# Optimization experiments

Hardware: AMD Instinct MI355X
Metric: run time of the kernel (lower is better)

Reference implementation:

```python
import jax, jax.numpy as jnp
import numpy as np

N, D_IN, D_HID, N_EXPERTS, TOP_K = 16384, 2048, 2048, 8, 2


def setup_inputs() -> dict:
    key = jax.random.key(0)
    k1, k2, k3, k4, k5 = jax.random.split(key, 5)
    x = jax.random.normal(k1, (N, D_IN), dtype=jnp.float32)
    W_experts = jax.random.normal(k2, (N_EXPERTS, D_IN, D_HID), dtype=jnp.float32) * 0.02
    b_experts = jax.random.normal(k3, (N_EXPERTS, D_HID), dtype=jnp.float32) * 0.02
    W_gate = jax.random.normal(k4, (D_IN, N_EXPERTS), dtype=jnp.float32) * 0.02
    b_gate = jax.random.normal(k5, (N_EXPERTS,), dtype=jnp.float32) * 0.02
    return {"x": x, "W_experts": W_experts, "b_experts": b_experts,
            "W_gate": W_gate, "b_gate": b_gate}


def reference(x, W_experts, b_experts, W_gate, b_gate):
    # gating softmax over experts: [N, E]
    gates = jax.nn.softmax(x @ W_gate + b_gate, axis=-1)
    # per-token top-k scores/indices: [N, K]
    top_scores, top_idx = jax.lax.top_k(gates, TOP_K)
    # FAITHFUL to original: experts chosen by the FIRST token's indices for all tokens
    idx0 = top_idx[0]                       # [K]
    W_sel = W_experts[idx0]                 # [K, D_IN, D_HID]
    b_sel = b_experts[idx0]                 # [K, D_HID]
    expert_out = jnp.einsum('ni,kio->nko', x, W_sel) + b_sel[None]  # [N, K, D_HID]
    # weight by each token's own top-k scores and sum over the K experts
    return (expert_out * top_scores[:, :, None]).sum(axis=1)        # [N, D_HID]
```

## Files before the change

kernel.cpp:

```cpp
#include <hip/hip_runtime.h>
#include <hip/hip_bf16.h>
#include <stdint.h>

#define N_TOK 16384
#define D_IN  2048
#define D_HID 2048

typedef __attribute__((ext_vector_type(8))) short  bf16x8;
typedef __attribute__((ext_vector_type(4))) float  f32x4;
typedef __attribute__((ext_vector_type(8))) unsigned short u16x8;

__device__ __forceinline__ unsigned short f2bf(float f) {
    unsigned int u = __float_as_uint(f);
    u = (u + 0x7FFFu + ((u >> 16) & 1u)) >> 16;
    return (unsigned short)u;
}

__global__ void gate_kernel(const float* __restrict__ x,
                            const float* __restrict__ Wg,
                            const float* __restrict__ bg,
                            float* __restrict__ s12,
                            int* __restrict__ eidx) {
    const int token = blockIdx.x * 4 + (threadIdx.x >> 6);
    const int lane  = threadIdx.x & 63;
    const float* xr = x + (size_t)token * D_IN;

    float acc[8];
#pragma unroll
    for (int e = 0; e < 8; ++e) acc[e] = 0.f;

    for (int i = lane; i < D_IN; i += 64) {
        float xv = xr[i];
        const float4* wr = (const float4*)(Wg + (size_t)i * 8);
        float4 w0 = wr[0], w1 = wr[1];
        acc[0] += xv * w0.x; acc[1] += xv * w0.y;
        acc[2] += xv * w0.z; acc[3] += xv * w0.w;
        acc[4] += xv * w1.x; acc[5] += xv * w1.y;
        acc[6] += xv * w1.z; acc[7] += xv * w1.w;
    }
#pragma unroll
    for (int off = 32; off > 0; off >>= 1) {
#pragma unroll
        for (int e = 0; e < 8; ++e) acc[e] += __shfl_xor(acc[e], off);
    }

    float lg[8];
    float mx = -1e30f;
#pragma unroll
    for (int e = 0; e < 8; ++e) { lg[e] = acc[e] + bg[e]; mx = fmaxf(mx, lg[e]); }
    float sum = 0.f;
#pragma unroll
    for (int e = 0; e < 8; ++e) { lg[e] = expf(lg[e] - mx); sum += lg[e]; }
    float inv = 1.f / sum;

    float s1 = -1.f, s2 = -1.f; int i1 = 0, i2 = 0;
#pragma unroll
    for (int e = 0; e < 8; ++e) {
        float g = lg[e] * inv;
        if (g > s1)      { s2 = s1; i2 = i1; s1 = g; i1 = e; }
        else if (g > s2) { s2 = g;  i2 = e; }
    }
    if (lane == 0) {
        s12[token * 2]     = s1;
        s12[token * 2 + 1] = s2;
        if (token == 0) { eidx[0] = i1; eidx[1] = i2; }
    }
}

__global__ __launch_bounds__(256) void xconv_kernel(
    const float* __restrict__ x, unsigned short* __restrict__ xb) {
    const int mt = blockIdx.x >> 6;
    const int kt = blockIdx.x & 63;
    const int t  = threadIdx.x;
    const float* src = x + ((size_t)(mt * 256 + t)) * D_IN + kt * 32;
    unsigned short* slab = xb + ((size_t)(mt * 64 + kt)) * 8192;
#pragma unroll
    for (int ks = 0; ks < 4; ++ks) {
        float4 a = *(const float4*)(src + ks * 8);
        float4 b = *(const float4*)(src + ks * 8 + 4);
        u16x8 v;
        v[0] = f2bf(a.x); v[1] = f2bf(a.y); v[2] = f2bf(a.z); v[3] = f2bf(a.w);
        v[4] = f2bf(b.x); v[5] = f2bf(b.y); v[6] = f2bf(b.z); v[7] = f2bf(b.w);
        *(u16x8*)(slab + (ks * 256 + t) * 8) = v;
    }
}

__global__ void wconv_kernel(const float* __restrict__ W,
                             const int* __restrict__ eidx,
                             unsigned short* __restrict__ wbT) {
    __shared__ float tile[64][65];
    const int be  = blockIdx.z;
    const int e   = eidx[be];
    const int k0  = blockIdx.y * 64;
    const int n0  = blockIdx.x * 64;
    const int bx  = n0 >> 7;
    const int cl0 = n0 & 127;
    const int kt0 = k0 >> 5;
    const float* src = W + (size_t)e * D_IN * D_HID;
    const int t = threadIdx.x;

#pragma unroll
    for (int p = 0; p < 4; ++p) {
        int row = p * 16 + (t >> 4);
        int col = (t & 15) * 4;
        const float* s = src + (size_t)(k0 + row) * D_HID + n0 + col;
        tile[row][col]     = s[0];
        tile[row][col + 1] = s[1];
        tile[row][col + 2] = s[2];
        tile[row][col + 3] = s[3];
    }
    __syncthreads();

    const int g   = (t >> 5) * 8;
    const int ktl = t >> 7;
    const int ks  = (t >> 5) & 3;
#pragma unroll
    for (int p = 0; p < 2; ++p) {
        int n = p * 32 + (t & 31);
        u16x8 v;
#pragma unroll
        for (int j = 0; j < 8; ++j) v[j] = f2bf(tile[g + j][n]);
        unsigned short* dst = wbT + ((size_t)(bx * 64 + kt0 + ktl)) * 8192 +
                              ((size_t)(ks * 256 + be * 128 + cl0 + n)) * 8;
        *(u16x8*)dst = v;
    }
}

#define GLD16(gp, lp)                                                        \
    __builtin_amdgcn_global_load_lds(                                        \
        (const __attribute__((address_space(1))) void*)(gp),                 \
        (__attribute__((address_space(3))) void*)(lp), 16, 0, 0)

#define LDSV(SLOT) (*(const bf16x8*)&lds[(SLOT) * 8])

#define STAGE_A(SBAS, KT)                                                    \
    do {                                                                     \
        GLD16(gA0 + (size_t)(KT) * 8192,        &lds[((SBAS) + t512) * 8]);  \
        GLD16(gA0 + (size_t)(KT) * 8192 + 4096, &lds[((SBAS) + 512 + t512) * 8]); \
    } while (0)
#define STAGE_B(SBAS, KT)                                                    \
    do {                                                                     \
        GLD16(gB0 + (size_t)(KT) * 8192,        &lds[((SBAS) + 1024 + t512) * 8]); \
        GLD16(gB0 + (size_t)(KT) * 8192 + 4096, &lds[((SBAS) + 1536 + t512) * 8]); \
    } while (0)

#define MF(MI, AV)                                                                              \
    acc[MI][0] = __builtin_amdgcn_mfma_f32_16x16x32_bf16(AV, bf0, acc[MI][0], 0, 0, 0);         \
    acc[MI][1] = __builtin_amdgcn_mfma_f32_16x16x32_bf16(AV, bf1, acc[MI][1], 0, 0, 0);         \
    acc[MI][2] = __builtin_amdgcn_mfma_f32_16x16x32_bf16(AV, bf2, acc[MI][2], 0, 0, 0);         \
    acc[MI][3] = __builtin_amdgcn_mfma_f32_16x16x32_bf16(AV, bf3, acc[MI][3], 0, 0, 0);

#define TILE(RB, SB, KT, DO_STAGE, VMSTR)                                    \
    do {                                                                     \
        const int rbas  = (RB) * 2048;                                       \
        const int abase = rbas + aks + arow;                                 \
        const int bbase = rbas + 1024 + aks + brow;                          \
        bf16x8 bf0 = LDSV(bbase), bf1 = LDSV(bbase + 16),                    \
               bf2 = LDSV(bbase + 32), bf3 = LDSV(bbase + 48);               \
        bf16x8 a0 = LDSV(abase), a1 = LDSV(abase + 16),                      \
               a2 = LDSV(abase + 32), a3 = LDSV(abase + 48);                 \
        bf16x8 a4 = LDSV(abase + 64), a5 = LDSV(abase + 80),                 \
               a6 = LDSV(abase + 96), a7 = LDSV(abase + 112);                \
        __builtin_amdgcn_s_barrier();                                        \
        if (DO_STAGE) STAGE_A((SB) * 2048, KT);                              \
        __builtin_amdgcn_s_setprio(1);                                       \
        MF(0, a0) MF(1, a1) MF(2, a2) MF(3, a3)                              \
        __builtin_amdgcn_s_setprio(0);                                       \
        asm volatile(VMSTR ::: "memory");                                    \
        __builtin_amdgcn_s_barrier();                                        \
        if (DO_STAGE) STAGE_B((SB) * 2048, KT);                              \
        __builtin_amdgcn_s_setprio(1);                                       \
        MF(4, a4) MF(5, a5) MF(6, a6) MF(7, a7)                              \
        __builtin_amdgcn_s_setprio(0);                                       \
    } while (0)

__global__ __launch_bounds__(512, 2) void moe_gemm_kernel(
    const unsigned short* __restrict__ xb,
    const unsigned short* __restrict__ wbT,
    const float* __restrict__ b_exp,
    const int* __restrict__ eidx,
    const float* __restrict__ s12,
    float* __restrict__ out) {
    __shared__ __align__(16) short lds[4 * 2048 * 8];

    const int t512 = threadIdx.x;
    const int lane = t512 & 63;
    const int w    = t512 >> 6;
    const int wm   = w >> 2;
    const int wn   = w & 3;

    const int bid = blockIdx.x;
    const int xcd = bid & 7;
    const int jb  = bid >> 3;
    const int bx  = xcd * 2 + (jb & 1);
    const int by  = jb >> 1;
    const int mbase = by * 256;
    const int nbase = bx * 128;

    const unsigned short* gA0 = xb  + ((size_t)by * 64) * 8192 + t512 * 8;
    const unsigned short* gB0 = wbT + ((size_t)bx * 64) * 8192 + t512 * 8;

    const int aks  = (lane >> 4) * 256;
    const int arow = wm * 128 + (lane & 15);
    const int brow = wn * 64 + (lane & 15);

    f32x4 acc[8][4];
#pragma unroll
    for (int mi = 0; mi < 8; ++mi)
#pragma unroll
        for (int ni = 0; ni < 4; ++ni) acc[mi][ni] = (f32x4){0.f, 0.f, 0.f, 0.f};

    STAGE_A(0, 0);    STAGE_B(0, 0);
    STAGE_A(2048, 1); STAGE_B(2048, 1);
    STAGE_A(4096, 2); STAGE_B(4096, 2);
    asm volatile("s_waitcnt vmcnt(8)" ::: "memory");
    __builtin_amdgcn_s_barrier();

#pragma unroll 4
    for (int t = 0; t < 61; ++t) {
        TILE(t & 3, (t + 3) & 3, t + 3, 1, "s_waitcnt vmcnt(6)");
    }
    TILE(1, 0, 0, 0, "s_waitcnt vmcnt(4)");
    TILE(2, 0, 0, 0, "s_waitcnt vmcnt(0)");
    TILE(3, 0, 0, 0, "s_waitcnt vmcnt(0)");

    __syncthreads();
    float* fl = (float*)lds;
    if (wn >= 2) {
        float* reg = fl + (wm * 2 + (wn - 2)) * 8192;
#pragma unroll
        for (int mi = 0; mi < 8; ++mi)
#pragma unroll
            for (int ni = 0; ni < 4; ++ni)
#pragma unroll
                for (int j = 0; j < 4; ++j) {
                    int row_l = mi * 16 + ((lane >> 4) << 2) + j;
                    int col_l = ni * 16 + (lane & 15);
                    reg[row_l * 64 + col_l] = acc[mi][ni][j];
                }
    }
    __syncthreads();
    if (wn < 2) {
        const float* reg = fl + (wm * 2 + wn) * 8192;
        const int e0 = eidx[0], e1 = eidx[1];
        const float* bb0 = b_exp + (size_t)e0 * D_HID;
        const float* bb1 = b_exp + (size_t)e1 * D_HID;
        const float2* s12v = (const float2*)s12;
        int   cc[4];
        float b0c[4], b1c[4];
#pragma unroll
        for (int ni = 0; ni < 4; ++ni) {
            cc[ni]  = nbase + wn * 64 + ni * 16 + (lane & 15);
            b0c[ni] = bb0[cc[ni]];
            b1c[ni] = bb1[cc[ni]];
        }
#pragma unroll
        for (int mi = 0; mi < 8; ++mi)
#pragma unroll
            for (int j = 0; j < 4; ++j) {
                int row_l = mi * 16 + ((lane >> 4) << 2) + j;
                int r = mbase + wm * 128 + row_l;
                float2 s = s12v[r];
#pragma unroll
                for (int ni = 0; ni < 4; ++ni) {
                    float y1 = reg[row_l * 64 + ni * 16 + (lane & 15)];
                    out[(size_t)r * D_HID + cc[ni]] =
                        s.x * (acc[mi][ni][j] + b0c[ni]) + s.y * (y1 + b1c[ni]);
                }
            }
    }
}

extern "C" void kernel_launch(void* const* d_in, const int* in_sizes, int n_in,
                              void* d_out, int out_size, void* d_ws, size_t ws_size,
                              hipStream_t stream) {
    const float* x         = (const float*)d_in[0];
    const float* W_experts = (const float*)d_in[1];
    const float* b_experts = (const float*)d_in[2];
    const float* W_gate    = (const float*)d_in[3];
    const float* b_gate    = (const float*)d_in[4];
    float* out = (float*)d_out;

    char* ws = (char*)d_ws;
    float* s12  = (float*)ws;
    int*   eidx = (int*)(ws + 131072);
    unsigned short* xb  = (unsigned short*)(ws + 262144);
    unsigned short* wbT = (unsigned short*)(ws + 262144 + 67108864);

    gate_kernel<<<N_TOK / 4, 256, 0, stream>>>(x, W_gate, b_gate, s12, eidx);
    xconv_kernel<<<4096, 256, 0, stream>>>(x, xb);
    wconv_kernel<<<dim3(32, 32, 2), 256, 0, stream>>>(W_experts, eidx, wbT);
    moe_gemm_kernel<<<1024, 512, 0, stream>>>(xb, wbT, b_experts, eidx, s12, out);
}
```

Before: 323.0 us.

## Software-pipeline LDS fragment loads across K-tiles with one barrier per tile

Restructures the GEMM main loop so the A/B fragment reads for the next K-tile are issued from LDS during the current tile's second MFMA phase, with double-buffered register sets. The per-tile barriers drop from two to one, and each phase issues its global staging before its MFMA block. The aim is to hide LDS read latency and barrier stalls behind MFMA work. The cost is more live VGPRs, which at 512 threads with two blocks per CU may cause spills. The tighter vmcnt and barrier ordering also risks races on LDS slot reuse.

```diff
diff --git a/kernel.cpp b/kernel.cpp
--- a/kernel.cpp
+++ b/kernel.cpp
@@ -144,34 +144,44 @@
         GLD16(gB0 + (size_t)(KT) * 8192 + 4096, &lds[((SBAS) + 1536 + t512) * 8]); \
     } while (0)
 
-#define MF(MI, AV)                                                                              \
-    acc[MI][0] = __builtin_amdgcn_mfma_f32_16x16x32_bf16(AV, bf0, acc[MI][0], 0, 0, 0);         \
-    acc[MI][1] = __builtin_amdgcn_mfma_f32_16x16x32_bf16(AV, bf1, acc[MI][1], 0, 0, 0);         \
-    acc[MI][2] = __builtin_amdgcn_mfma_f32_16x16x32_bf16(AV, bf2, acc[MI][2], 0, 0, 0);         \
-    acc[MI][3] = __builtin_amdgcn_mfma_f32_16x16x32_bf16(AV, bf3, acc[MI][3], 0, 0, 0);
-
-#define TILE(RB, SB, KT, DO_STAGE, VMSTR)                                    \
+#define MF16(ASET, BSET, MB)                                                 \
+    _Pragma("unroll")                                                        \
+    for (int mi = 0; mi < 4; ++mi)                                           \
+        _Pragma("unroll")                                                    \
+        for (int ni = 0; ni < 4; ++ni)                                       \
+            acc[(MB) + mi][ni] = __builtin_amdgcn_mfma_f32_16x16x32_bf16(    \
+                ASET[mi], BSET[ni], acc[(MB) + mi][ni], 0, 0, 0);
+
+#define PH1(TT, STG, AS, BS)                                                 \
     do {                                                                     \
-        const int rbas  = (RB) * 2048;                                       \
-        const int abase = rbas + aks + arow;                                 \
-        const int bbase = rbas + 1024 + aks + brow;                          \
-        bf16x8 bf0 = LDSV(bbase), bf1 = LDSV(bbase + 16),                    \
-               bf2 = LDSV(bbase + 32), bf3 = LDSV(bbase + 48);               \
-        bf16x8 a0 = LDSV(abase), a1 = LDSV(abase + 16),                      \
-               a2 = LDSV(abase + 32), a3 = LDSV(abase + 48);                 \
-        bf16x8 a4 = LDSV(abase + 64), a5 = LDSV(abase + 80),                 \
-               a6 = LDSV(abase + 96), a7 = LDSV(abase + 112);                \
+        const int rb = ((TT) & 3) * 2048;                                    \
+        a4[0] = LDSV(rb + aks + arow + 64);                                  \
+        a4[1] = LDSV(rb + aks + arow + 80);                                  \
+        a4[2] = LDSV(rb + aks + arow + 96);                                  \
+        a4[3] = LDSV(rb + aks + arow + 112);                                 \
+        if (STG) STAGE_A((((TT) + 3) & 3) * 2048, (TT) + 3);                 \
+        __builtin_amdgcn_s_setprio(1);                                       \
+        MF16(AS, BS, 0)                                                      \
+        __builtin_amdgcn_s_setprio(0);                                       \
+    } while (0)
+
+#define PH2(TT, STG, VMSTR, BN, AN, BC)                                      \
+    do {                                                                     \
+        const int rb = (((TT) + 1) & 3) * 2048;                              \
+        BN[0] = LDSV(rb + 1024 + aks + brow);                                \
+        BN[1] = LDSV(rb + 1024 + aks + brow + 16);                           \
+        BN[2] = LDSV(rb + 1024 + aks + brow + 32);                           \
+        BN[3] = LDSV(rb + 1024 + aks + brow + 48);                           \
+        AN[0] = LDSV(rb + aks + arow);                                       \
+        AN[1] = LDSV(rb + aks + arow + 16);                                  \
+        AN[2] = LDSV(rb + aks + arow + 32);                                  \
+        AN[3] = LDSV(rb + aks + arow + 48);                                  \
+        if (STG) STAGE_B((((TT) + 3) & 3) * 2048, (TT) + 3);                 \
+        asm volatile(VMSTR ::: "memory");                                    \
+        __builtin_amdgcn_s_setprio(1);                                       \
+        MF16(a4, BC, 4)                                                      \
+        __builtin_amdgcn_s_setprio(0);                                       \
         __builtin_amdgcn_s_barrier();                                        \
-        if (DO_STAGE) STAGE_A((SB) * 2048, KT);                              \
-        __builtin_amdgcn_s_setprio(1);                                       \
-        MF(0, a0) MF(1, a1) MF(2, a2) MF(3, a3)                              \
-        __builtin_amdgcn_s_setprio(0);                                       \
-        asm volatile(VMSTR ::: "memory");                                    \
-        __builtin_amdgcn_s_barrier();                                        \
-        if (DO_STAGE) STAGE_B((SB) * 2048, KT);                              \
-        __builtin_amdgcn_s_setprio(1);                                       \
-        MF(4, a4) MF(5, a5) MF(6, a6) MF(7, a7)                              \
-        __builtin_amdgcn_s_setprio(0);                                       \
     } while (0)
 
 __global__ __launch_bounds__(512, 2) void moe_gemm_kernel(
@@ -210,19 +220,39 @@
 #pragma unroll
         for (int ni = 0; ni < 4; ++ni) acc[mi][ni] = (f32x4){0.f, 0.f, 0.f, 0.f};
 
+    bf16x8 bA[4], a0A[4], bB[4], a0B[4], a4[4];
+
     STAGE_A(0, 0);    STAGE_B(0, 0);
     STAGE_A(2048, 1); STAGE_B(2048, 1);
     STAGE_A(4096, 2); STAGE_B(4096, 2);
-    asm volatile("s_waitcnt vmcnt(8)" ::: "memory");
+    asm volatile("s_waitcnt vmcnt(4)" ::: "memory");
     __builtin_amdgcn_s_barrier();
-
-#pragma unroll 4
-    for (int t = 0; t < 61; ++t) {
-        TILE(t & 3, (t + 3) & 3, t + 3, 1, "s_waitcnt vmcnt(6)");
-    }
-    TILE(1, 0, 0, 0, "s_waitcnt vmcnt(4)");
-    TILE(2, 0, 0, 0, "s_waitcnt vmcnt(0)");
-    TILE(3, 0, 0, 0, "s_waitcnt vmcnt(0)");
+    bA[0] = LDSV(1024 + aks + brow);      bA[1] = LDSV(1024 + aks + brow + 16);
+    bA[2] = LDSV(1024 + aks + brow + 32); bA[3] = LDSV(1024 + aks + brow + 48);
+    a0A[0] = LDSV(aks + arow);            a0A[1] = LDSV(aks + arow + 16);
+    a0A[2] = LDSV(aks + arow + 32);       a0A[3] = LDSV(aks + arow + 48);
+
+    for (int t = 0; t < 60; t += 2) {
+        PH1(t, 1, a0A, bA);
+        PH2(t, 1, "s_waitcnt vmcnt(4)", bB, a0B, bA);
+        PH1(t + 1, 1, a0B, bB);
+        PH2(t + 1, 1, "s_waitcnt vmcnt(4)", bA, a0A, bB);
+    }
+    PH1(60, 1, a0A, bA);
+    PH2(60, 1, "s_waitcnt vmcnt(4)", bB, a0B, bA);
+    PH1(61, 0, a0B, bB);
+    PH2(61, 0, "s_waitcnt vmcnt(0)", bA, a0A, bB);
+    PH1(62, 0, a0A, bA);
+    PH2(62, 0, "s_waitcnt vmcnt(0)", bB, a0B, bA);
+    {
+        const int rb = 3 * 2048;
+        a4[0] = LDSV(rb + aks + arow + 64);
+        a4[1] = LDSV(rb + aks + arow + 80);
+        a4[2] = LDSV(rb + aks + arow + 96);
+        a4[3] = LDSV(rb + aks + arow + 112);
+        MF16(a0B, bB, 0)
+        MF16(a4, bB, 4)
+    }
 
     __syncthreads();
     float* fl = (float*)lds;
```

After: 329.1 us. Within noise of the previous version (+1.9%).

## Restructure GEMM main loop into double-buffered four-phase pipeline

Applied to the files above, without the earlier changes.

Replaces the four-slot LDS ring of k-tiles with a double buffer of two-k-tile chunks, processed in four phases per iteration. Each phase loads a quarter of the A fragments (B fragments every other phase), issues the global-to-LDS prefetch for the matching slice of the next chunk, then runs 16 MFMAs behind a barrier and an explicit lgkmcnt wait. The aim is to spread LDS reads and global loads more evenly between MFMA bursts and to cut register pressure from holding eight A fragments at once. In exchange there are more barriers per k-tile and the prefetch distance is shorter than the previous three-tile lookahead.

```diff
diff --git a/kernel.cpp b/kernel.cpp
--- a/kernel.cpp
+++ b/kernel.cpp
@@ -133,45 +133,41 @@
 
 #define LDSV(SLOT) (*(const bf16x8*)&lds[(SLOT) * 8])
 
-#define STAGE_A(SBAS, KT)                                                    \
+#define PHASE(CB, P, T1, DOSTAGE, VMSTR)                                     \
     do {                                                                     \
-        GLD16(gA0 + (size_t)(KT) * 8192,        &lds[((SBAS) + t512) * 8]);  \
-        GLD16(gA0 + (size_t)(KT) * 8192 + 4096, &lds[((SBAS) + 512 + t512) * 8]); \
-    } while (0)
-#define STAGE_B(SBAS, KT)                                                    \
-    do {                                                                     \
-        GLD16(gB0 + (size_t)(KT) * 8192,        &lds[((SBAS) + 1024 + t512) * 8]); \
-        GLD16(gB0 + (size_t)(KT) * 8192 + 4096, &lds[((SBAS) + 1536 + t512) * 8]); \
-    } while (0)
-
-#define MF(MI, AV)                                                                              \
-    acc[MI][0] = __builtin_amdgcn_mfma_f32_16x16x32_bf16(AV, bf0, acc[MI][0], 0, 0, 0);         \
-    acc[MI][1] = __builtin_amdgcn_mfma_f32_16x16x32_bf16(AV, bf1, acc[MI][1], 0, 0, 0);         \
-    acc[MI][2] = __builtin_amdgcn_mfma_f32_16x16x32_bf16(AV, bf2, acc[MI][2], 0, 0, 0);         \
-    acc[MI][3] = __builtin_amdgcn_mfma_f32_16x16x32_bf16(AV, bf3, acc[MI][3], 0, 0, 0);
-
-#define TILE(RB, SB, KT, DO_STAGE, VMSTR)                                    \
-    do {                                                                     \
-        const int rbas  = (RB) * 2048;                                       \
-        const int abase = rbas + aks + arow;                                 \
-        const int bbase = rbas + 1024 + aks + brow;                          \
-        bf16x8 bf0 = LDSV(bbase), bf1 = LDSV(bbase + 16),                    \
-               bf2 = LDSV(bbase + 32), bf3 = LDSV(bbase + 48);               \
-        bf16x8 a0 = LDSV(abase), a1 = LDSV(abase + 16),                      \
-               a2 = LDSV(abase + 32), a3 = LDSV(abase + 48);                 \
-        bf16x8 a4 = LDSV(abase + 64), a5 = LDSV(abase + 80),                 \
-               a6 = LDSV(abase + 96), a7 = LDSV(abase + 112);                \
+        const int hb = (CB) * 4096 + ((P) >> 1) * 2048;                      \
+        if (((P) & 1) == 0) {                                                \
+            bC[0] = LDSV(hb + 1024 + bro);                                   \
+            bC[1] = LDSV(hb + 1024 + bro + 16);                              \
+            bC[2] = LDSV(hb + 1024 + bro + 32);                              \
+            bC[3] = LDSV(hb + 1024 + bro + 48);                              \
+        }                                                                    \
+        aP[0] = LDSV(hb + aro + ((P) & 1) * 64);                             \
+        aP[1] = LDSV(hb + aro + ((P) & 1) * 64 + 16);                        \
+        aP[2] = LDSV(hb + aro + ((P) & 1) * 64 + 32);                        \
+        aP[3] = LDSV(hb + aro + ((P) & 1) * 64 + 48);                        \
+        if (DOSTAGE) {                                                       \
+            const size_t so = ((size_t)(2 * (T1) + ((P) >> 1)) * 1024 +      \
+                               ((P) & 1) * 512) * 8;                         \
+            const int dd = ((CB) ^ 1) * 4096 + ((P) >> 1) * 2048 +           \
+                           ((P) & 1) * 512 + t512;                           \
+            GLD16(gA0 + so, &lds[dd * 8]);                                   \
+            GLD16(gB0 + so, &lds[(dd + 1024) * 8]);                          \
+        }                                                                    \
+        if (VMSTR[0]) asm volatile(VMSTR ::: "memory");                      \
         __builtin_amdgcn_s_barrier();                                        \
-        if (DO_STAGE) STAGE_A((SB) * 2048, KT);                              \
+        asm volatile("s_waitcnt lgkmcnt(0)" ::: "memory");                   \
+        __builtin_amdgcn_sched_barrier(0);                                   \
         __builtin_amdgcn_s_setprio(1);                                       \
-        MF(0, a0) MF(1, a1) MF(2, a2) MF(3, a3)                              \
+        _Pragma("unroll")                                                    \
+        for (int mi = 0; mi < 4; ++mi)                                       \
+            _Pragma("unroll")                                                \
+            for (int ni = 0; ni < 4; ++ni)                                   \
+                acc[((P) & 1) * 4 + mi][ni] =                                \
+                    __builtin_amdgcn_mfma_f32_16x16x32_bf16(                 \
+                        aP[mi], bC[ni], acc[((P) & 1) * 4 + mi][ni], 0, 0, 0); \
         __builtin_amdgcn_s_setprio(0);                                       \
-        asm volatile(VMSTR ::: "memory");                                    \
         __builtin_amdgcn_s_barrier();                                        \
-        if (DO_STAGE) STAGE_B((SB) * 2048, KT);                              \
-        __builtin_amdgcn_s_setprio(1);                                       \
-        MF(4, a4) MF(5, a5) MF(6, a6) MF(7, a7)                              \
-        __builtin_amdgcn_s_setprio(0);                                       \
     } while (0)
 
 __global__ __launch_bounds__(512, 2) void moe_gemm_kernel(
@@ -181,7 +177,7 @@
     const int* __restrict__ eidx,
     const float* __restrict__ s12,
     float* __restrict__ out) {
-    __shared__ __align__(16) short lds[4 * 2048 * 8];
+    __shared__ __align__(16) short lds[2 * 4096 * 8];
 
     const int t512 = threadIdx.x;
     const int lane = t512 & 63;
@@ -200,9 +196,8 @@
     const unsigned short* gA0 = xb  + ((size_t)by * 64) * 8192 + t512 * 8;
     const unsigned short* gB0 = wbT + ((size_t)bx * 64) * 8192 + t512 * 8;
 
-    const int aks  = (lane >> 4) * 256;
-    const int arow = wm * 128 + (lane & 15);
-    const int brow = wn * 64 + (lane & 15);
+    const int aro = (lane >> 4) * 256 + wm * 128 + (lane & 15);
+    const int bro = (lane >> 4) * 256 + wn * 64 + (lane & 15);
 
     f32x4 acc[8][4];
 #pragma unroll
@@ -210,19 +205,30 @@
 #pragma unroll
         for (int ni = 0; ni < 4; ++ni) acc[mi][ni] = (f32x4){0.f, 0.f, 0.f, 0.f};
 
-    STAGE_A(0, 0);    STAGE_B(0, 0);
-    STAGE_A(2048, 1); STAGE_B(2048, 1);
-    STAGE_A(4096, 2); STAGE_B(4096, 2);
-    asm volatile("s_waitcnt vmcnt(8)" ::: "memory");
+    bf16x8 aP[4], bC[4];
+
+#pragma unroll
+    for (int p = 0; p < 4; ++p) {
+        const size_t so = ((size_t)(p >> 1) * 1024 + (p & 1) * 512) * 8;
+        const int dd = (p >> 1) * 2048 + (p & 1) * 512 + t512;
+        GLD16(gA0 + so, &lds[dd * 8]);
+        GLD16(gB0 + so, &lds[(dd + 1024) * 8]);
+    }
+    asm volatile("s_waitcnt vmcnt(4)" ::: "memory");
     __builtin_amdgcn_s_barrier();
 
-#pragma unroll 4
-    for (int t = 0; t < 61; ++t) {
-        TILE(t & 3, (t + 3) & 3, t + 3, 1, "s_waitcnt vmcnt(6)");
-    }
-    TILE(1, 0, 0, 0, "s_waitcnt vmcnt(4)");
-    TILE(2, 0, 0, 0, "s_waitcnt vmcnt(0)");
-    TILE(3, 0, 0, 0, "s_waitcnt vmcnt(0)");
+    int cb = 0;
+    for (int t = 0; t < 31; ++t) {
+        PHASE(cb, 0, t + 1, 1, "");
+        PHASE(cb, 1, t + 1, 1, "s_waitcnt vmcnt(4)");
+        PHASE(cb, 2, t + 1, 1, "");
+        PHASE(cb, 3, t + 1, 1, "s_waitcnt vmcnt(4)");
+        cb ^= 1;
+    }
+    PHASE(1, 0, 0, 0, "");
+    PHASE(1, 1, 0, 0, "s_waitcnt vmcnt(0)");
+    PHASE(1, 2, 0, 0, "");
+    PHASE(1, 3, 0, 0, "");
 
     __syncthreads();
     float* fl = (float*)lds;
```

Measured after the change: 341.4 us. 1.06x slower.

## Load B fragments directly into registers, staging only A through LDS

Applied to the files above, without the earlier changes.

The GEMM main loop now streams only the A (token) tile through LDS with async global-to-LDS loads. Each wave loads its B (weight) fragments straight from global memory into registers, double-buffered one k-tile ahead. This halves LDS traffic and usage per stage and replaces two barriers per tile with one. The cost is more register pressure, per-wave redundant global loads of B across the wm waves, and reliance on carefully tuned vmcnt waits for correctness.

```diff
diff --git a/kernel.cpp b/kernel.cpp
--- a/kernel.cpp
+++ b/kernel.cpp
@@ -133,46 +133,38 @@
 
 #define LDSV(SLOT) (*(const bf16x8*)&lds[(SLOT) * 8])
 
-#define STAGE_A(SBAS, KT)                                                    \
+#define STAGE_A(SB, KT)                                                      \
     do {                                                                     \
-        GLD16(gA0 + (size_t)(KT) * 8192,        &lds[((SBAS) + t512) * 8]);  \
-        GLD16(gA0 + (size_t)(KT) * 8192 + 4096, &lds[((SBAS) + 512 + t512) * 8]); \
+        GLD16(gA0 + (size_t)(KT) * 8192,        &lds[((SB) * 1024 + t512) * 8]); \
+        GLD16(gA0 + (size_t)(KT) * 8192 + 4096, &lds[((SB) * 1024 + 512 + t512) * 8]); \
     } while (0)
-#define STAGE_B(SBAS, KT)                                                    \
+
+#define TILE(RB, STGT, DOSTG, BT, DOB, BC, BN, VMSTR, DOBAR)                 \
     do {                                                                     \
-        GLD16(gB0 + (size_t)(KT) * 8192,        &lds[((SBAS) + 1024 + t512) * 8]); \
-        GLD16(gB0 + (size_t)(KT) * 8192 + 4096, &lds[((SBAS) + 1536 + t512) * 8]); \
+        bf16x8 a[8];                                                         \
+        _Pragma("unroll")                                                    \
+        for (int mi = 0; mi < 8; ++mi)                                       \
+            a[mi] = LDSV((RB) * 1024 + abase + mi * 16);                     \
+        if (DOB) {                                                           \
+            const unsigned short* bp = gBfrag + (size_t)(BT) * 8192;         \
+            _Pragma("unroll")                                                \
+            for (int ni = 0; ni < 4; ++ni)                                   \
+                BN[ni] = *(const bf16x8*)(bp + ni * 128);                    \
+        }                                                                    \
+        if (DOSTG) STAGE_A((STGT) & 3, STGT);                                \
+        if (VMSTR[0]) asm volatile(VMSTR ::: "memory");                      \
+        __builtin_amdgcn_s_setprio(1);                                       \
+        _Pragma("unroll")                                                    \
+        for (int mi = 0; mi < 8; ++mi)                                       \
+            _Pragma("unroll")                                                \
+            for (int ni = 0; ni < 4; ++ni)                                   \
+                acc[mi][ni] = __builtin_amdgcn_mfma_f32_16x16x32_bf16(       \
+                    a[mi], BC[ni], acc[mi][ni], 0, 0, 0);                    \
+        __builtin_amdgcn_s_setprio(0);                                       \
+        if (DOBAR) __builtin_amdgcn_s_barrier();                             \
     } while (0)
 
-#define MF(MI, AV)                                                                              \
-    acc[MI][0] = __builtin_amdgcn_mfma_f32_16x16x32_bf16(AV, bf0, acc[MI][0], 0, 0, 0);         \
-    acc[MI][1] = __builtin_amdgcn_mfma_f32_16x16x32_bf16(AV, bf1, acc[MI][1], 0, 0, 0);         \
-    acc[MI][2] = __builtin_amdgcn_mfma_f32_16x16x32_bf16(AV, bf2, acc[MI][2], 0, 0, 0);         \
-    acc[MI][3] = __builtin_amdgcn_mfma_f32_16x16x32_bf16(AV, bf3, acc[MI][3], 0, 0, 0);
-
-#define TILE(RB, SB, KT, DO_STAGE, VMSTR)                                    \
-    do {                                                                     \
-        const int rbas  = (RB) * 2048;                                       \
-        const int abase = rbas + aks + arow;                                 \
-        const int bbase = rbas + 1024 + aks + brow;                          \
-        bf16x8 bf0 = LDSV(bbase), bf1 = LDSV(bbase + 16),                    \
-               bf2 = LDSV(bbase + 32), bf3 = LDSV(bbase + 48);               \
-        bf16x8 a0 = LDSV(abase), a1 = LDSV(abase + 16),                      \
-               a2 = LDSV(abase + 32), a3 = LDSV(abase + 48);                 \
-        bf16x8 a4 = LDSV(abase + 64), a5 = LDSV(abase + 80),                 \
-               a6 = LDSV(abase + 96), a7 = LDSV(abase + 112);                \
-        __builtin_amdgcn_s_barrier();                                        \
-        if (DO_STAGE) STAGE_A((SB) * 2048, KT);                              \
-        __builtin_amdgcn_s_setprio(1);                                       \
-        MF(0, a0) MF(1, a1) MF(2, a2) MF(3, a3)                              \
-        __builtin_amdgcn_s_setprio(0);                                       \
-        asm volatile(VMSTR ::: "memory");                                    \
-        __builtin_amdgcn_s_barrier();                                        \
-        if (DO_STAGE) STAGE_B((SB) * 2048, KT);                              \
-        __builtin_amdgcn_s_setprio(1);                                       \
-        MF(4, a4) MF(5, a5) MF(6, a6) MF(7, a7)                              \
-        __builtin_amdgcn_s_setprio(0);                                       \
-    } while (0)
+#define VM12 "s_waitcnt vmcnt(12)"
 
 __global__ __launch_bounds__(512, 2) void moe_gemm_kernel(
     const unsigned short* __restrict__ xb,
@@ -181,7 +173,7 @@
     const int* __restrict__ eidx,
     const float* __restrict__ s12,
     float* __restrict__ out) {
-    __shared__ __align__(16) short lds[4 * 2048 * 8];
+    __shared__ __align__(16) short lds[8192 * 8];
 
     const int t512 = threadIdx.x;
     const int lane = t512 & 63;
@@ -197,12 +189,12 @@
     const int mbase = by * 256;
     const int nbase = bx * 128;
 
-    const unsigned short* gA0 = xb  + ((size_t)by * 64) * 8192 + t512 * 8;
-    const unsigned short* gB0 = wbT + ((size_t)bx * 64) * 8192 + t512 * 8;
-
-    const int aks  = (lane >> 4) * 256;
-    const int arow = wm * 128 + (lane & 15);
-    const int brow = wn * 64 + (lane & 15);
+    const unsigned short* gA0 = xb + ((size_t)by * 64) * 8192 + t512 * 8;
+    const unsigned short* gBfrag =
+        wbT + ((size_t)bx * 64) * 8192 +
+        ((size_t)((lane >> 4) * 256 + wn * 64 + (lane & 15))) * 8;
+
+    const int abase = (lane >> 4) * 256 + wm * 128 + (lane & 15);
 
     f32x4 acc[8][4];
 #pragma unroll
@@ -210,19 +202,31 @@
 #pragma unroll
         for (int ni = 0; ni < 4; ++ni) acc[mi][ni] = (f32x4){0.f, 0.f, 0.f, 0.f};
 
-    STAGE_A(0, 0);    STAGE_B(0, 0);
-    STAGE_A(2048, 1); STAGE_B(2048, 1);
-    STAGE_A(4096, 2); STAGE_B(4096, 2);
+    bf16x8 b0[4], b1[4];
+
+    STAGE_A(0, 0);
+    STAGE_A(1, 1);
+    STAGE_A(2, 2);
+#pragma unroll
+    for (int ni = 0; ni < 4; ++ni)
+        b0[ni] = *(const bf16x8*)(gBfrag + ni * 128);
     asm volatile("s_waitcnt vmcnt(8)" ::: "memory");
     __builtin_amdgcn_s_barrier();
 
-#pragma unroll 4
-    for (int t = 0; t < 61; ++t) {
-        TILE(t & 3, (t + 3) & 3, t + 3, 1, "s_waitcnt vmcnt(6)");
-    }
-    TILE(1, 0, 0, 0, "s_waitcnt vmcnt(4)");
-    TILE(2, 0, 0, 0, "s_waitcnt vmcnt(0)");
-    TILE(3, 0, 0, 0, "s_waitcnt vmcnt(0)");
+    for (int t = 0; t < 56; t += 4) {
+        TILE(0, t + 3, 1, t + 1, 1, b0, b1, VM12, 1);
+        TILE(1, t + 4, 1, t + 2, 1, b1, b0, VM12, 1);
+        TILE(2, t + 5, 1, t + 3, 1, b0, b1, VM12, 1);
+        TILE(3, t + 6, 1, t + 4, 1, b1, b0, VM12, 1);
+    }
+    TILE(0, 59, 1, 57, 1, b0, b1, VM12, 1);
+    TILE(1, 60, 1, 58, 1, b1, b0, VM12, 1);
+    TILE(2, 61, 1, 59, 1, b0, b1, VM12, 1);
+    TILE(3, 62, 1, 60, 1, b1, b0, VM12, 1);
+    TILE(0, 63, 1, 61, 1, b0, b1, VM12, 1);
+    TILE(1, 0, 0, 62, 1, b1, b0, "s_waitcnt vmcnt(10)", 1);
+    TILE(2, 0, 0, 63, 1, b0, b1, "s_waitcnt vmcnt(8)", 1);
+    TILE(3, 0, 0, 0, 0, b1, b0, "", 0);
 
     __syncthreads();
     float* fl = (float*)lds;
```

After: 349.2 us. +8.1%, slower.
